# Performance work log

Hardware: AMD Instinct MI355X
Metric: run time of the kernel (lower is better)

Reference implementation:

```python
import jax, jax.numpy as jnp
import numpy as np

B, L, D, H, U = 64, 1024, 1024, 1024, 1024

def setup_inputs() -> dict:
    key = jax.random.key(0)
    ks = jax.random.split(key, 6)
    scale = 0.02
    return {
        "features": jax.random.normal(ks[0], (B, L, D), jnp.float32),
        "hidden": jax.random.normal(ks[1], (B, H), jnp.float32),
        "W1": jax.random.normal(ks[2], (D, U), jnp.float32) * scale,
        "b1": jnp.zeros((U,), jnp.float32),
        "W2": jax.random.normal(ks[3], (H, U), jnp.float32) * scale,
        "b2": jnp.zeros((U,), jnp.float32),
        "V": jax.random.normal(ks[4], (U, 1), jnp.float32) * scale,
        "bV": jnp.zeros((1,), jnp.float32),
    }

def reference(features, hidden, W1, b1, W2, b2, V, bV):
    # features: [B, L, D], hidden: [B, H]
    proj_f = jnp.einsum("bld,du->blu", features, W1) + b1        # [B, L, U]
    proj_h = (hidden @ W2 + b2)[:, None, :]                        # [B, 1, U]
    score = jnp.tanh(proj_f + proj_h) @ V + bV                    # [B, L, 1]
    attention_weights = jax.nn.softmax(score, axis=1)             # [B, L, 1]
    context_vector = jnp.sum(attention_weights * features, axis=1)  # [B, D]
    return context_vector, attention_weights
```

## Files before the change

kernel.cpp:

```cpp
#include <hip/hip_runtime.h>


#define GLD16(g, l) __builtin_amdgcn_global_load_lds(                          \
    (const __attribute__((address_space(1))) void*)(g),                        \
    (__attribute__((address_space(3))) void*)(l), 16, 0, 0)

typedef __attribute__((ext_vector_type(8))) short bf16x8;
typedef __attribute__((ext_vector_type(4))) float f32x4;
typedef __attribute__((ext_vector_type(8))) unsigned short us8;

__device__ __forceinline__ unsigned short f2bf(float f) {
  unsigned u = __float_as_uint(f);
  return (unsigned short)((u + 0x7FFFu + ((u >> 16) & 1u)) >> 16);
}

__global__ __launch_bounds__(256) void projh_k(
    const float* __restrict__ hidden, const float* __restrict__ W2,
    const float* __restrict__ b2, float* __restrict__ ph) {
  __shared__ float hs[1024];
  __shared__ float red[4][64];
  const int b = blockIdx.y, ch = blockIdx.x, t = threadIdx.x;
#pragma unroll
  for (int j = 0; j < 4; ++j) hs[t + j * 256] = hidden[b * 1024 + t + j * 256];
  __syncthreads();
  const int ul = t & 63, hq = t >> 6;
  const int u = ch * 64 + ul;
  float acc = 0.f;
#pragma unroll 4
  for (int i = 0; i < 256; ++i) {
    int h = hq * 256 + i;
    acc += hs[h] * W2[(size_t)h * 1024 + u];
  }
  red[hq][ul] = acc;
  __syncthreads();
  if (t < 64) {
    float s = red[0][t] + red[1][t] + red[2][t] + red[3][t] + b2[ch * 64 + t];
    ph[b * 1024 + ch * 64 + t] = s;
  }
}

__global__ __launch_bounds__(256) void w1tile_k(
    const float* __restrict__ W1, unsigned short* __restrict__ w1t) {
  const int i = blockIdx.x * 256 + threadIdx.x;
  const int u = i >> 7, c = i & 127;
  const int ks = c >> 2, kg = c & 3;
  const int col = u & 127, nb = u >> 7;
  us8 pk;
#pragma unroll
  for (int j = 0; j < 8; ++j) {
    int d = ks * 32 + kg * 8 + j;
    pk[j] = f2bf(W1[(size_t)d * 1024 + u]);
  }
  size_t off = (size_t)(nb * 32 + ks) * 4096 + col * 32 +
               ((unsigned)(kg ^ (col & 3)) << 3);
  *(us8*)(&w1t[off]) = pk;
}

__global__ __launch_bounds__(256) void score_gemm(
    const float* __restrict__ feat, const unsigned short* __restrict__ w1t,
    const float* __restrict__ b1, const float* __restrict__ ph,
    const float* __restrict__ V, float* __restrict__ partial) {
  __shared__ unsigned short As[2][128 * 32];
  __shared__ unsigned short Bs[2][128 * 32];
  __shared__ float phb1_s[128], vs_s[128];
  __shared__ float red2[2][128];

  const int nb = blockIdx.x;
  const int m_base = blockIdx.y * 128;
  const int b = m_base >> 10;
  const int tid = threadIdx.x;
  const int lane = tid & 63;
  const int w = tid >> 6, wr = w >> 1, wc = w & 1;

  if (tid < 128) {
    int u = nb * 128 + tid;
    phb1_s[tid] = b1[u] + ph[b * 1024 + u];
    vs_s[tid] = V[u];
  }

  f32x4 acc[4][4];
#pragma unroll
  for (int mi = 0; mi < 4; ++mi)
#pragma unroll
    for (int ni = 0; ni < 4; ++ni) acc[mi][ni] = (f32x4){0.f, 0.f, 0.f, 0.f};

  const int srow = tid >> 3;
  const int scg = tid & 7;
  const float* fbase = feat + (size_t)m_base * 1024 + scg * 4;
  const unsigned short* wpanel = w1t + (size_t)nb * 131072;

  {
#pragma unroll
    for (int j = 0; j < 2; ++j) {
      int cch = w * 2 + j;
      GLD16(wpanel + cch * 512 + lane * 8, &Bs[0][cch * 512]);
    }
#pragma unroll
    for (int p = 0; p < 4; ++p) {
      int row = p * 32 + srow;
      float4 v = *(const float4*)(fbase + (size_t)row * 1024);
      int off = row * 32 + ((scg * 4) ^ ((row & 3) << 3));
      unsigned a0 = f2bf(v.x) | ((unsigned)f2bf(v.y) << 16);
      unsigned a1 = f2bf(v.z) | ((unsigned)f2bf(v.w) << 16);
      *(uint2*)(&As[0][off]) = make_uint2(a0, a1);
    }
  }
  __syncthreads();

  const int kg = lane >> 4;
  int aoff[4], boff[4];
#pragma unroll
  for (int mi = 0; mi < 4; ++mi) {
    int row = wr * 64 + mi * 16 + (lane & 15);
    aoff[mi] = row * 32 + ((kg * 8) ^ ((row & 3) << 3));
  }
#pragma unroll
  for (int ni = 0; ni < 4; ++ni) {
    int col = wc * 64 + ni * 16 + (lane & 15);
    boff[ni] = col * 32 + ((kg * 8) ^ ((col & 3) << 3));
  }

  int cur = 0;
  for (int ks = 0; ks < 32; ++ks) {
    const int nxt = cur ^ 1;
    const bool more = (ks + 1) < 32;
    float4 av[4];
    if (more) {
      const unsigned short* tsrc = wpanel + (size_t)(ks + 1) * 4096;
#pragma unroll
      for (int j = 0; j < 2; ++j) {
        int cch = w * 2 + j;
        GLD16(tsrc + cch * 512 + lane * 8, &Bs[nxt][cch * 512]);
      }
#pragma unroll
      for (int p = 0; p < 4; ++p) {
        int row = p * 32 + srow;
        av[p] = *(const float4*)(fbase + (size_t)row * 1024 + (ks + 1) * 32);
      }
    }
    bf16x8 afr[4], bfr[4];
#pragma unroll
    for (int mi = 0; mi < 4; ++mi)
      afr[mi] = *(const bf16x8*)(&As[cur][aoff[mi]]);
#pragma unroll
    for (int ni = 0; ni < 4; ++ni)
      bfr[ni] = *(const bf16x8*)(&Bs[cur][boff[ni]]);
#pragma unroll
    for (int mi = 0; mi < 4; ++mi)
#pragma unroll
      for (int ni = 0; ni < 4; ++ni)
        acc[mi][ni] = __builtin_amdgcn_mfma_f32_16x16x32_bf16(
            afr[mi], bfr[ni], acc[mi][ni], 0, 0, 0);
    if (more) {
#pragma unroll
      for (int p = 0; p < 4; ++p) {
        int row = p * 32 + srow;
        int off = row * 32 + ((scg * 4) ^ ((row & 3) << 3));
        unsigned a0 = f2bf(av[p].x) | ((unsigned)f2bf(av[p].y) << 16);
        unsigned a1 = f2bf(av[p].z) | ((unsigned)f2bf(av[p].w) << 16);
        *(uint2*)(&As[nxt][off]) = make_uint2(a0, a1);
      }
    }
    __syncthreads();
    cur = nxt;
  }

  float rs[4][4];
#pragma unroll
  for (int mi = 0; mi < 4; ++mi)
#pragma unroll
    for (int r = 0; r < 4; ++r) rs[mi][r] = 0.f;
#pragma unroll
  for (int ni = 0; ni < 4; ++ni) {
    int ucol = wc * 64 + ni * 16 + (lane & 15);
    float pv = phb1_s[ucol], vv = vs_s[ucol];
#pragma unroll
    for (int mi = 0; mi < 4; ++mi)
#pragma unroll
      for (int r = 0; r < 4; ++r)
        rs[mi][r] += tanhf(acc[mi][ni][r] + pv) * vv;
  }
#pragma unroll
  for (int mi = 0; mi < 4; ++mi)
#pragma unroll
    for (int r = 0; r < 4; ++r) {
      float x = rs[mi][r];
      x += __shfl_xor(x, 1);
      x += __shfl_xor(x, 2);
      x += __shfl_xor(x, 4);
      x += __shfl_xor(x, 8);
      rs[mi][r] = x;
    }
  if ((lane & 15) == 0) {
    int rq = lane >> 4;
#pragma unroll
    for (int mi = 0; mi < 4; ++mi)
#pragma unroll
      for (int r = 0; r < 4; ++r)
        red2[wc][wr * 64 + mi * 16 + rq * 4 + r] = rs[mi][r];
  }
  __syncthreads();
  if (tid < 128)
    partial[(size_t)nb * 65536 + m_base + tid] = red2[0][tid] + red2[1][tid];
}

__global__ __launch_bounds__(256) void softmax_k(
    const float* __restrict__ partial, float* __restrict__ wout) {
  const int b = blockIdx.x, t = threadIdx.x;
  const int lane = t & 63, w = t >> 6;
  __shared__ float smax[4], ssum[4];
  float s[4];
#pragma unroll
  for (int j = 0; j < 4; ++j) {
    int l = t + j * 256;
    float v = 0.f;
#pragma unroll
    for (int nb = 0; nb < 8; ++nb) v += partial[(size_t)nb * 65536 + b * 1024 + l];
    s[j] = v;
  }
  float mx = fmaxf(fmaxf(s[0], s[1]), fmaxf(s[2], s[3]));
#pragma unroll
  for (int off = 1; off < 64; off <<= 1) mx = fmaxf(mx, __shfl_xor(mx, off));
  if (lane == 0) smax[w] = mx;
  __syncthreads();
  mx = fmaxf(fmaxf(smax[0], smax[1]), fmaxf(smax[2], smax[3]));
  float e[4], sum = 0.f;
#pragma unroll
  for (int j = 0; j < 4; ++j) { e[j] = expf(s[j] - mx); sum += e[j]; }
#pragma unroll
  for (int off = 1; off < 64; off <<= 1) sum += __shfl_xor(sum, off);
  if (lane == 0) ssum[w] = sum;
  __syncthreads();
  const float inv = 1.f / (ssum[0] + ssum[1] + ssum[2] + ssum[3]);
#pragma unroll
  for (int j = 0; j < 4; ++j) wout[b * 1024 + t + j * 256] = e[j] * inv;
}

__global__ __launch_bounds__(256) void context_k(
    const float* __restrict__ feat, const float* __restrict__ wts,
    float* __restrict__ ctx) {
  __shared__ float wsm[1024];
  __shared__ float red[128];
  const int b = blockIdx.y, ch = blockIdx.x, t = threadIdx.x;
#pragma unroll
  for (int j = 0; j < 4; ++j) wsm[t + j * 256] = wts[b * 1024 + t + j * 256];
  __syncthreads();
  const int dl = t & 127, lh = t >> 7;
  const int d = ch * 128 + dl;
  const float* fb = feat + (size_t)b * 1048576 + d;
  float acc = 0.f;
#pragma unroll 4
  for (int l = lh * 512; l < lh * 512 + 512; ++l)
    acc += wsm[l] * fb[(size_t)l * 1024];
  if (lh == 0) red[dl] = acc;
  __syncthreads();
  if (lh == 1) ctx[b * 1024 + d] = red[dl] + acc;
}

extern "C" void kernel_launch(void* const* d_in, const int* in_sizes, int n_in,
                              void* d_out, int out_size, void* d_ws,
                              size_t ws_size, hipStream_t stream) {
  const float* feat = (const float*)d_in[0];
  const float* hidden = (const float*)d_in[1];
  const float* W1 = (const float*)d_in[2];
  const float* b1 = (const float*)d_in[3];
  const float* W2 = (const float*)d_in[4];
  const float* b2 = (const float*)d_in[5];
  const float* V = (const float*)d_in[6];
  float* out = (float*)d_out;

  float* ph = (float*)d_ws;
  float* partial = ph + 65536;
  unsigned short* w1t = (unsigned short*)(partial + 524288);

  hipLaunchKernelGGL(projh_k, dim3(16, 64), dim3(256), 0, stream, hidden, W2, b2, ph);
  hipLaunchKernelGGL(w1tile_k, dim3(512), dim3(256), 0, stream, W1, w1t);
  hipLaunchKernelGGL(score_gemm, dim3(8, 512), dim3(256), 0, stream, feat, w1t, b1, ph, V, partial);
  hipLaunchKernelGGL(softmax_k, dim3(64), dim3(256), 0, stream, partial, out + 65536);
  hipLaunchKernelGGL(context_k, dim3(8, 64), dim3(256), 0, stream, feat, out + 65536, out);
}
```

Baseline: 877.9 us.

## Pre-convert features to bf16 MFMA fragment layout and stream both GEMM operands via LDS DMA

Adds a pass that converts the fp32 features once into a bf16 buffer laid out in MFMA fragment order, and rewrites W1 tiling into the same fragment order. The GEMM then loads both operands with direct global-to-LDS loads and reads fragments contiguously, with no in-loop conversion or swizzle. Blocks are remapped so the 8 N-panels sharing an M tile run near each other for L2 reuse. The cost is an extra full read of features plus a 128MB bf16 write and reread. A fallback keeps the old path when the workspace is too small.

```diff
diff --git a/kernel.cpp b/kernel.cpp
--- a/kernel.cpp
+++ b/kernel.cpp
@@ -39,7 +39,144 @@
   }
 }
 
-__global__ __launch_bounds__(256) void w1tile_k(
+
+__global__ __launch_bounds__(256) void w1tile_frag_k(
+    const float* __restrict__ W1, unsigned short* __restrict__ w1t) {
+  const int i = blockIdx.x * 256 + threadIdx.x;
+  const int l = i & 63, nt = (i >> 6) & 7, ks = (i >> 9) & 31, nb = i >> 14;
+  const int kg = l >> 4, c = l & 15;
+  const int u = nb * 128 + nt * 16 + c;
+  us8 pk;
+#pragma unroll
+  for (int j = 0; j < 8; ++j)
+    pk[j] = f2bf(W1[(size_t)(ks * 32 + kg * 8 + j) * 1024 + u]);
+  *(us8*)(&w1t[(size_t)i * 8]) = pk;
+}
+
+__global__ __launch_bounds__(256) void featconv_k(
+    const float* __restrict__ feat, unsigned short* __restrict__ featb) {
+  const int i = blockIdx.x * 256 + threadIdx.x;
+  const int l = i & 63, mt = (i >> 6) & 7, ks = (i >> 9) & 31, mb = i >> 14;
+  const int row = mb * 128 + mt * 16 + (l & 15);
+  const int k = ks * 32 + (l >> 4) * 8;
+  const float* p = feat + (size_t)row * 1024 + k;
+  float4 a = *(const float4*)p;
+  float4 b = *(const float4*)(p + 4);
+  us8 pk;
+  pk[0] = f2bf(a.x); pk[1] = f2bf(a.y); pk[2] = f2bf(a.z); pk[3] = f2bf(a.w);
+  pk[4] = f2bf(b.x); pk[5] = f2bf(b.y); pk[6] = f2bf(b.z); pk[7] = f2bf(b.w);
+  *(us8*)(&featb[(size_t)i * 8]) = pk;
+}
+
+__global__ __launch_bounds__(256) void score_gemm(
+    const unsigned short* __restrict__ featb,
+    const unsigned short* __restrict__ w1t, const float* __restrict__ b1,
+    const float* __restrict__ ph, const float* __restrict__ V,
+    float* __restrict__ partial) {
+  __shared__ unsigned short As[2][4096];
+  __shared__ unsigned short Bs[2][4096];
+  __shared__ float phb1_s[128], vs_s[128];
+  __shared__ float red2[2][128];
+
+  const int nb = blockIdx.y & 7;
+  const int mb = ((blockIdx.y >> 3) << 3) + blockIdx.x;
+  const int m_base = mb * 128;
+  const int b = m_base >> 10;
+  const int tid = threadIdx.x;
+  const int lane = tid & 63;
+  const int w = tid >> 6, wr = w >> 1, wc = w & 1;
+
+  if (tid < 128) {
+    int u = nb * 128 + tid;
+    phb1_s[tid] = b1[u] + ph[b * 1024 + u];
+    vs_s[tid] = V[u];
+  }
+
+  f32x4 acc[4][4];
+#pragma unroll
+  for (int mi = 0; mi < 4; ++mi)
+#pragma unroll
+    for (int ni = 0; ni < 4; ++ni) acc[mi][ni] = (f32x4){0.f, 0.f, 0.f, 0.f};
+
+  const unsigned short* Asrc = featb + (size_t)mb * 131072;
+  const unsigned short* Bsrc = w1t + (size_t)nb * 131072;
+
+#define STAGE(ksv, buf)                                                        \
+  {                                                                            \
+    _Pragma("unroll") for (int p = 0; p < 2; ++p) {                            \
+      int mt = w * 2 + p;                                                      \
+      GLD16(Asrc + ((size_t)(ksv) * 8 + mt) * 512 + lane * 8,                  \
+            &As[buf][mt * 512]);                                               \
+      GLD16(Bsrc + ((size_t)(ksv) * 8 + mt) * 512 + lane * 8,                  \
+            &Bs[buf][mt * 512]);                                               \
+    }                                                                          \
+  }
+
+  STAGE(0, 0);
+  __syncthreads();
+
+  int cur = 0;
+  for (int ks = 0; ks < 32; ++ks) {
+    const int nxt = cur ^ 1;
+    if (ks + 1 < 32) STAGE(ks + 1, nxt);
+    bf16x8 afr[4], bfr[4];
+#pragma unroll
+    for (int mi = 0; mi < 4; ++mi)
+      afr[mi] = *(const bf16x8*)(&As[cur][(wr * 4 + mi) * 512 + lane * 8]);
+#pragma unroll
+    for (int ni = 0; ni < 4; ++ni)
+      bfr[ni] = *(const bf16x8*)(&Bs[cur][(wc * 4 + ni) * 512 + lane * 8]);
+#pragma unroll
+    for (int mi = 0; mi < 4; ++mi)
+#pragma unroll
+      for (int ni = 0; ni < 4; ++ni)
+        acc[mi][ni] = __builtin_amdgcn_mfma_f32_16x16x32_bf16(
+            afr[mi], bfr[ni], acc[mi][ni], 0, 0, 0);
+    __syncthreads();
+    cur = nxt;
+  }
+#undef STAGE
+
+  float rs[4][4];
+#pragma unroll
+  for (int mi = 0; mi < 4; ++mi)
+#pragma unroll
+    for (int r = 0; r < 4; ++r) rs[mi][r] = 0.f;
+#pragma unroll
+  for (int ni = 0; ni < 4; ++ni) {
+    int ucol = wc * 64 + ni * 16 + (lane & 15);
+    float pv = phb1_s[ucol], vv = vs_s[ucol];
+#pragma unroll
+    for (int mi = 0; mi < 4; ++mi)
+#pragma unroll
+      for (int r = 0; r < 4; ++r)
+        rs[mi][r] += tanhf(acc[mi][ni][r] + pv) * vv;
+  }
+#pragma unroll
+  for (int mi = 0; mi < 4; ++mi)
+#pragma unroll
+    for (int r = 0; r < 4; ++r) {
+      float x = rs[mi][r];
+      x += __shfl_xor(x, 1);
+      x += __shfl_xor(x, 2);
+      x += __shfl_xor(x, 4);
+      x += __shfl_xor(x, 8);
+      rs[mi][r] = x;
+    }
+  if ((lane & 15) == 0) {
+    int rq = lane >> 4;
+#pragma unroll
+    for (int mi = 0; mi < 4; ++mi)
+#pragma unroll
+      for (int r = 0; r < 4; ++r)
+        red2[wc][wr * 64 + mi * 16 + rq * 4 + r] = rs[mi][r];
+  }
+  __syncthreads();
+  if (tid < 128)
+    partial[(size_t)nb * 65536 + m_base + tid] = red2[0][tid] + red2[1][tid];
+}
+
+__global__ __launch_bounds__(256) void w1tile_fb_k(
     const float* __restrict__ W1, unsigned short* __restrict__ w1t) {
   const int i = blockIdx.x * 256 + threadIdx.x;
   const int u = i >> 7, c = i & 127;
@@ -56,7 +193,7 @@
   *(us8*)(&w1t[off]) = pk;
 }
 
-__global__ __launch_bounds__(256) void score_gemm(
+__global__ __launch_bounds__(256) void score_fb_k(
     const float* __restrict__ feat, const unsigned short* __restrict__ w1t,
     const float* __restrict__ b1, const float* __restrict__ ph,
     const float* __restrict__ V, float* __restrict__ partial) {
@@ -64,31 +201,26 @@
   __shared__ unsigned short Bs[2][128 * 32];
   __shared__ float phb1_s[128], vs_s[128];
   __shared__ float red2[2][128];
-
   const int nb = blockIdx.x;
   const int m_base = blockIdx.y * 128;
   const int b = m_base >> 10;
   const int tid = threadIdx.x;
   const int lane = tid & 63;
   const int w = tid >> 6, wr = w >> 1, wc = w & 1;
-
   if (tid < 128) {
     int u = nb * 128 + tid;
     phb1_s[tid] = b1[u] + ph[b * 1024 + u];
     vs_s[tid] = V[u];
   }
-
   f32x4 acc[4][4];
 #pragma unroll
   for (int mi = 0; mi < 4; ++mi)
 #pragma unroll
     for (int ni = 0; ni < 4; ++ni) acc[mi][ni] = (f32x4){0.f, 0.f, 0.f, 0.f};
-
   const int srow = tid >> 3;
   const int scg = tid & 7;
   const float* fbase = feat + (size_t)m_base * 1024 + scg * 4;
   const unsigned short* wpanel = w1t + (size_t)nb * 131072;
-
   {
 #pragma unroll
     for (int j = 0; j < 2; ++j) {
@@ -106,7 +238,6 @@
     }
   }
   __syncthreads();
-
   const int kg = lane >> 4;
   int aoff[4], boff[4];
 #pragma unroll
@@ -119,7 +250,6 @@
     int col = wc * 64 + ni * 16 + (lane & 15);
     boff[ni] = col * 32 + ((kg * 8) ^ ((col & 3) << 3));
   }
-
   int cur = 0;
   for (int ks = 0; ks < 32; ++ks) {
     const int nxt = cur ^ 1;
@@ -164,7 +294,6 @@
     __syncthreads();
     cur = nxt;
   }
-
   float rs[4][4];
 #pragma unroll
   for (int mi = 0; mi < 4; ++mi)
@@ -272,10 +401,18 @@
   float* ph = (float*)d_ws;
   float* partial = ph + 65536;
   unsigned short* w1t = (unsigned short*)(partial + 524288);
+  unsigned short* featb = w1t + 1048576;
+  const size_t need = 4456448ull + 134217728ull;
 
   hipLaunchKernelGGL(projh_k, dim3(16, 64), dim3(256), 0, stream, hidden, W2, b2, ph);
-  hipLaunchKernelGGL(w1tile_k, dim3(512), dim3(256), 0, stream, W1, w1t);
-  hipLaunchKernelGGL(score_gemm, dim3(8, 512), dim3(256), 0, stream, feat, w1t, b1, ph, V, partial);
+  if (ws_size >= need) {
+    hipLaunchKernelGGL(w1tile_frag_k, dim3(512), dim3(256), 0, stream, W1, w1t);
+    hipLaunchKernelGGL(featconv_k, dim3(32768), dim3(256), 0, stream, feat, featb);
+    hipLaunchKernelGGL(score_gemm, dim3(8, 512), dim3(256), 0, stream, featb, w1t, b1, ph, V, partial);
+  } else {
+    hipLaunchKernelGGL(w1tile_fb_k, dim3(512), dim3(256), 0, stream, W1, w1t);
+    hipLaunchKernelGGL(score_fb_k, dim3(8, 512), dim3(256), 0, stream, feat, w1t, b1, ph, V, partial);
+  }
   hipLaunchKernelGGL(softmax_k, dim3(64), dim3(256), 0, stream, partial, out + 65536);
   hipLaunchKernelGGL(context_k, dim3(8, 64), dim3(256), 0, stream, feat, out + 65536, out);
 }
```

New measurement: 783.9 us. -10.7%, faster.
